# Performance work log

Hardware: AMD Instinct MI355X
Metric: run time of the kernel (lower is better)

Reference implementation:

```python
import jax, jax.numpy as jnp
import numpy as np

BATCH = 4096
NUM_INPUTS = 784
WIDTH = 16000        # neurons per logic layer, divisible by NUM_CLASSES
N_HIDDEN = 4         # width->width layers stacked for scan (plus the input layer)
NUM_CLASSES = 10


def setup_inputs() -> dict:
    key = jax.random.key(0)
    ks = jax.random.split(key, 7)
    x = jax.random.bernoulli(ks[0], 0.5, (BATCH, NUM_INPUTS))
    idx_a0 = jax.random.randint(ks[1], (WIDTH,), 0, NUM_INPUTS, dtype=jnp.int32)
    idx_b0 = jax.random.randint(ks[2], (WIDTH,), 0, NUM_INPUTS, dtype=jnp.int32)
    neg0 = jax.random.bernoulli(ks[3], 0.5, (WIDTH, 2))
    idx_a = jax.random.randint(ks[4], (N_HIDDEN, WIDTH), 0, WIDTH, dtype=jnp.int32)
    idx_b = jax.random.randint(ks[5], (N_HIDDEN, WIDTH), 0, WIDTH, dtype=jnp.int32)
    neg = jax.random.bernoulli(ks[6], 0.5, (N_HIDDEN, WIDTH, 2))
    return {"x": x, "idx_a0": idx_a0, "idx_b0": idx_b0, "neg0": neg0,
            "idx_a": idx_a, "idx_b": idx_b, "neg": neg}


def _gate(a, b, nf):
    # gate = (maybe-NOT a) AND (maybe-NOT b); NOT on booleans == XOR with flag
    return (a ^ nf[:, 0]) & (b ^ nf[:, 1])


def reference(x, idx_a0, idx_b0, neg0, idx_a, idx_b, neg):
    # input layer: gather wires from the boolean input
    h = _gate(x[:, idx_a0], x[:, idx_b0], neg0)  # [BATCH, WIDTH] bool

    def step(h, p):
        ia, ib, nf = p
        return _gate(h[:, ia], h[:, ib], nf), None

    h, _ = jax.lax.scan(step, h, (idx_a, idx_b, neg))
    # GroupSum: popcount per class group -> int32 logits
    out = h.reshape(BATCH, NUM_CLASSES, WIDTH // NUM_CLASSES).sum(-1, dtype=jnp.int32)
    return out
```

## Files before the change

kernel.cpp:

```cpp
#include <hip/hip_runtime.h>


#define NIN   784
#define WIDTH 16000
#define SW    16384
#define NH    4
#define NC    10
#define GPC   1600
#define NBLK  128
#define TPB   1024

typedef unsigned int u32;

__launch_bounds__(TPB, 4)
__global__ void net_kernel(const int* __restrict__ x,
                           const int* __restrict__ ia0, const int* __restrict__ ib0,
                           const int* __restrict__ n0,
                           const int* __restrict__ iah, const int* __restrict__ ibh,
                           const int* __restrict__ nh,
                           int* __restrict__ out) {
    __shared__ __align__(16) u32 xw[NIN];
    __shared__ __align__(16) u32 bufA[SW];
    __shared__ __align__(16) u32 bufB[SW];

    int w = blockIdx.x;
    int t = threadIdx.x;

    if (t < NIN) {
        const int* base = x + (size_t)(w * 32) * NIN + t;
        u32 acc = 0;
#pragma unroll
        for (int r = 0; r < 32; ++r)
            acc |= (base[(size_t)r * NIN] != 0 ? 1u : 0u) << r;
        xw[t] = acc;
    }
    __syncthreads();

    int i3 = t + 3 * TPB; if (i3 > 3999) i3 = 3999;

    u32* cur = xw;
#pragma unroll
    for (int l = 0; l <= NH; ++l) {
        u32* dst = (l & 1) ? bufB : bufA;
        const int* pa = l ? iah + (size_t)(l - 1) * WIDTH : ia0;
        const int* pb = l ? ibh + (size_t)(l - 1) * WIDTH : ib0;
        const int* pn = l ? nh  + (size_t)(l - 1) * 2 * WIDTH : n0;

        uint4 ta[2], tb[2];
        uint4 rn0[3], rn1[3];
        u32 av[12], bv[12];

#define IDX(S) ((S) == 3 ? i3 : (t + (S) * TPB))

#define LOADRAW(S, B, SLOT) { \
        int ii = IDX(S); \
        ta[B]  = *(const uint4*)(pa + 4 * ii); \
        tb[B]  = *(const uint4*)(pb + 4 * ii); \
        rn0[SLOT] = *(const uint4*)(pn + 8 * ii); \
        rn1[SLOT] = *(const uint4*)(pn + 8 * ii + 4); }

#define ISSUE(B, SLOT) { \
        av[4*(SLOT)+0] = cur[(u32)ta[B].x]; bv[4*(SLOT)+0] = cur[(u32)tb[B].x]; \
        av[4*(SLOT)+1] = cur[(u32)ta[B].y]; bv[4*(SLOT)+1] = cur[(u32)tb[B].y]; \
        av[4*(SLOT)+2] = cur[(u32)ta[B].z]; bv[4*(SLOT)+2] = cur[(u32)tb[B].z]; \
        av[4*(SLOT)+3] = cur[(u32)ta[B].w]; bv[4*(SLOT)+3] = cur[(u32)tb[B].w]; }

#define CONSUME(S, SLOT) { \
        uint4 r; \
        r.x = (av[4*(SLOT)+0] ^ (0u - (u32)(rn0[SLOT].x != 0))) & (bv[4*(SLOT)+0] ^ (0u - (u32)(rn0[SLOT].y != 0))); \
        r.y = (av[4*(SLOT)+1] ^ (0u - (u32)(rn0[SLOT].z != 0))) & (bv[4*(SLOT)+1] ^ (0u - (u32)(rn0[SLOT].w != 0))); \
        r.z = (av[4*(SLOT)+2] ^ (0u - (u32)(rn1[SLOT].x != 0))) & (bv[4*(SLOT)+2] ^ (0u - (u32)(rn1[SLOT].y != 0))); \
        r.w = (av[4*(SLOT)+3] ^ (0u - (u32)(rn1[SLOT].z != 0))) & (bv[4*(SLOT)+3] ^ (0u - (u32)(rn1[SLOT].w != 0))); \
        *(uint4*)(dst + 4 * (t + (S) * TPB)) = r; }

        LOADRAW(0, 0, 0);
        LOADRAW(1, 1, 1);
        ISSUE(0, 0);
        LOADRAW(2, 0, 2);
        ISSUE(1, 1);
        CONSUME(0, 0);
        LOADRAW(3, 1, 0);
        ISSUE(0, 2);
        CONSUME(1, 1);
        ISSUE(1, 0);
        CONSUME(2, 2);
        CONSUME(3, 0);

#undef LOADRAW
#undef ISSUE
#undef CONSUME
#undef IDX

        __syncthreads();
        cur = dst;
    }
    u32* res = bufA;

    int wave = t >> 6, lane = t & 63;
    if (wave < NC) {
        int c = wave;
        const u32* base = res + c * GPC;
        u32 p0 = 0, p1 = 0, p2 = 0, p3 = 0, p4 = 0;
#define CSA5(VAL) { u32 cy = (VAL); u32 s; \
        s = p0; p0 = s ^ cy; cy = s & cy; \
        s = p1; p1 = s ^ cy; cy = s & cy; \
        s = p2; p2 = s ^ cy; cy = s & cy; \
        s = p3; p3 = s ^ cy; cy = s & cy; \
        s = p4; p4 = s ^ cy; }
#pragma unroll
        for (int k = 0; k < 6; ++k) {
            uint4 v = *(const uint4*)(base + 4 * lane + 256 * k);
            CSA5(v.x); CSA5(v.y); CSA5(v.z); CSA5(v.w);
        }
        CSA5(base[1536 + lane]);
#undef CSA5

        u32 pl[11];
        pl[0] = p0; pl[1] = p1; pl[2] = p2; pl[3] = p3; pl[4] = p4;
#pragma unroll
        for (int s = 0; s < 6; ++s) {
            int np = 5 + s;
            u32 q[11];
#pragma unroll
            for (int i = 0; i < 11; ++i) if (i < np) q[i] = __shfl_xor(pl[i], 1 << s, 64);
            u32 carry = 0;
#pragma unroll
            for (int i = 0; i < 11; ++i) if (i < np) {
                u32 a = pl[i], b = q[i];
                u32 xr = a ^ b;
                pl[i] = xr ^ carry;
                carry = (a & b) | (carry & xr);
            }
            pl[np] = carry;
        }

        if (lane < 32) {
            int cntv = 0;
#pragma unroll
            for (int i = 0; i < 11; ++i) cntv += (int)((pl[i] >> lane) & 1u) << i;
            out[((size_t)w * 32 + lane) * NC + c] = cntv;
        }
    }
}

extern "C" void kernel_launch(void* const* d_in, const int* in_sizes, int n_in,
                              void* d_out, int out_size, void* d_ws, size_t ws_size,
                              hipStream_t stream) {
    const int* x      = (const int*)d_in[0];
    const int* idx_a0 = (const int*)d_in[1];
    const int* idx_b0 = (const int*)d_in[2];
    const int* neg0   = (const int*)d_in[3];
    const int* idx_a  = (const int*)d_in[4];
    const int* idx_b  = (const int*)d_in[5];
    const int* neg    = (const int*)d_in[6];
    int* out = (int*)d_out;

    (void)d_ws; (void)ws_size;

    net_kernel<<<NBLK, TPB, 0, stream>>>(
        x, idx_a0, idx_b0, neg0, idx_a, idx_b, neg, out);
}
```

Before: 86.28 us.

## Prefetch next layer's wiring indices across barriers and predicate the tail chunk

Issues the first two chunks of wiring-index and negation loads for each layer before the previous layer's barrier, so those global loads overlap the input bit-packing and the previous layer's compute. Register slots rotate across layers to hold the prefetched data. The fourth chunk is now skipped for threads past the real width instead of clamped to a duplicate index, which removes redundant loads and stores. This raises register pressure, which could affect occupancy at 1024 threads per block.

After: 86.71 us. No clear change (+0.5%).

```diff
diff --git a/kernel.cpp b/kernel.cpp
--- a/kernel.cpp
+++ b/kernel.cpp
@@ -25,39 +25,18 @@
 
     int w = blockIdx.x;
     int t = threadIdx.x;
+    const bool p3 = (t < 928);
 
-    if (t < NIN) {
-        const int* base = x + (size_t)(w * 32) * NIN + t;
-        u32 acc = 0;
-#pragma unroll
-        for (int r = 0; r < 32; ++r)
-            acc |= (base[(size_t)r * NIN] != 0 ? 1u : 0u) << r;
-        xw[t] = acc;
-    }
-    __syncthreads();
+    uint4 ta[2], tb[2];
+    uint4 rn0[3], rn1[3];
+    u32 av[12], bv[12];
 
-    int i3 = t + 3 * TPB; if (i3 > 3999) i3 = 3999;
-
-    u32* cur = xw;
-#pragma unroll
-    for (int l = 0; l <= NH; ++l) {
-        u32* dst = (l & 1) ? bufB : bufA;
-        const int* pa = l ? iah + (size_t)(l - 1) * WIDTH : ia0;
-        const int* pb = l ? ibh + (size_t)(l - 1) * WIDTH : ib0;
-        const int* pn = l ? nh  + (size_t)(l - 1) * 2 * WIDTH : n0;
-
-        uint4 ta[2], tb[2];
-        uint4 rn0[3], rn1[3];
-        u32 av[12], bv[12];
-
-#define IDX(S) ((S) == 3 ? i3 : (t + (S) * TPB))
-
-#define LOADRAW(S, B, SLOT) { \
-        int ii = IDX(S); \
-        ta[B]  = *(const uint4*)(pa + 4 * ii); \
-        tb[B]  = *(const uint4*)(pb + 4 * ii); \
-        rn0[SLOT] = *(const uint4*)(pn + 8 * ii); \
-        rn1[SLOT] = *(const uint4*)(pn + 8 * ii + 4); }
+#define LOADRAW(PA, PB, PN, II, B, SLOT) { \
+        int ii = (II); \
+        ta[B]     = *(const uint4*)((PA) + 4 * ii); \
+        tb[B]     = *(const uint4*)((PB) + 4 * ii); \
+        rn0[SLOT] = *(const uint4*)((PN) + 8 * ii); \
+        rn1[SLOT] = *(const uint4*)((PN) + 8 * ii + 4); }
 
 #define ISSUE(B, SLOT) { \
         av[4*(SLOT)+0] = cur[(u32)ta[B].x]; bv[4*(SLOT)+0] = cur[(u32)tb[B].x]; \
@@ -73,40 +52,64 @@
         r.w = (av[4*(SLOT)+3] ^ (0u - (u32)(rn1[SLOT].z != 0))) & (bv[4*(SLOT)+3] ^ (0u - (u32)(rn1[SLOT].w != 0))); \
         *(uint4*)(dst + 4 * (t + (S) * TPB)) = r; }
 
-        LOADRAW(0, 0, 0);
-        LOADRAW(1, 1, 1);
-        ISSUE(0, 0);
-        LOADRAW(2, 0, 2);
-        ISSUE(1, 1);
-        CONSUME(0, 0);
-        LOADRAW(3, 1, 0);
-        ISSUE(0, 2);
-        CONSUME(1, 1);
-        ISSUE(1, 0);
-        CONSUME(2, 2);
-        CONSUME(3, 0);
+    LOADRAW(ia0, ib0, n0, t,       0, 0);
+    LOADRAW(ia0, ib0, n0, t + TPB, 1, 1);
 
+    if (t < NIN) {
+        const int* base = x + (size_t)(w * 32) * NIN + t;
+        u32 acc = 0;
+#pragma unroll
+        for (int r = 0; r < 32; ++r)
+            acc |= (base[(size_t)r * NIN] != 0 ? 1u : 0u) << r;
+        xw[t] = acc;
+    }
+    __syncthreads();
+
+    u32* cur = xw;
+#pragma unroll
+    for (int l = 0; l <= NH; ++l) {
+        u32* dst = (l & 1) ? bufB : bufA;
+        const int sp = l % 3, sq = (l + 1) % 3, sr = (l + 2) % 3;
+        const int* pa = l ? iah + (size_t)(l - 1) * WIDTH     : ia0;
+        const int* pb = l ? ibh + (size_t)(l - 1) * WIDTH     : ib0;
+        const int* pn = l ? nh  + (size_t)(l - 1) * 2 * WIDTH : n0;
+
+        ISSUE(0, sp);
+        LOADRAW(pa, pb, pn, t + 2 * TPB, 0, sr);
+        ISSUE(1, sq);
+        CONSUME(0, sp);
+        if (p3) LOADRAW(pa, pb, pn, t + 3 * TPB, 1, sp);
+        ISSUE(0, sr);
+        CONSUME(1, sq);
+        if (p3) ISSUE(1, sp);
+        CONSUME(2, sr);
+        if (l < NH) {
+            const int* qa = iah + (size_t)l * WIDTH;
+            const int* qb = ibh + (size_t)l * WIDTH;
+            const int* qn = nh  + (size_t)l * 2 * WIDTH;
+            LOADRAW(qa, qb, qn, t,       0, sq);
+            LOADRAW(qa, qb, qn, t + TPB, 1, sr);
+        }
+        if (p3) CONSUME(3, sp);
+        __syncthreads();
+        cur = dst;
+    }
 #undef LOADRAW
 #undef ISSUE
 #undef CONSUME
-#undef IDX
-
-        __syncthreads();
-        cur = dst;
-    }
     u32* res = bufA;
 
     int wave = t >> 6, lane = t & 63;
     if (wave < NC) {
         int c = wave;
         const u32* base = res + c * GPC;
-        u32 p0 = 0, p1 = 0, p2 = 0, p3 = 0, p4 = 0;
+        u32 p0 = 0, p1 = 0, p2 = 0, p3v = 0, p4 = 0;
 #define CSA5(VAL) { u32 cy = (VAL); u32 s; \
-        s = p0; p0 = s ^ cy; cy = s & cy; \
-        s = p1; p1 = s ^ cy; cy = s & cy; \
-        s = p2; p2 = s ^ cy; cy = s & cy; \
-        s = p3; p3 = s ^ cy; cy = s & cy; \
-        s = p4; p4 = s ^ cy; }
+        s = p0;  p0  = s ^ cy; cy = s & cy; \
+        s = p1;  p1  = s ^ cy; cy = s & cy; \
+        s = p2;  p2  = s ^ cy; cy = s & cy; \
+        s = p3v; p3v = s ^ cy; cy = s & cy; \
+        s = p4;  p4  = s ^ cy; }
 #pragma unroll
         for (int k = 0; k < 6; ++k) {
             uint4 v = *(const uint4*)(base + 4 * lane + 256 * k);
@@ -116,7 +119,7 @@
 #undef CSA5
 
         u32 pl[11];
-        pl[0] = p0; pl[1] = p1; pl[2] = p2; pl[3] = p3; pl[4] = p4;
+        pl[0] = p0; pl[1] = p1; pl[2] = p2; pl[3] = p3v; pl[4] = p4;
 #pragma unroll
         for (int s = 0; s < 6; ++s) {
             int np = 5 + s;
```
